# Optimization experiments

Measured on AMD Instinct MI355X. Metric: run time of the kernel, lower is better.

Reference implementation:

```python
import jax, jax.numpy as jnp
import numpy as np

N_NODES = 50000
N_EDGES = 800000
GEN_EPS = 1e-7
LN_EPS = 1e-5


def _mlp3_tanh(x, w0, b0, w1, b1, w2, b2):
    x = jnp.tanh(x @ w0.T + b0)
    x = jnp.tanh(x @ w1.T + b1)
    return jnp.tanh(x @ w2.T + b2)


def _gen_conv(x, src, dst, edge_attr, w0, b0, ln_w, ln_b, w1, b1):
    # GENConv(aggr='softmax', t=1): msg = relu(x_j + e) + eps
    msg = jax.nn.relu(x[src] + edge_attr) + GEN_EPS          # [E, 64]
    m = jax.ops.segment_max(msg, dst, num_segments=N_NODES)  # [N, 64]
    ex = jnp.exp(msg - m[dst])
    den = jax.ops.segment_sum(ex, dst, num_segments=N_NODES)
    alpha = ex / den[dst]                                    # scatter-softmax per dst
    agg = jax.ops.segment_sum(alpha * msg, dst, num_segments=N_NODES)
    h = x + agg                                              # x_r + aggregated messages
    # internal MLP: Linear(64->128), LayerNorm(128), ReLU, Linear(128->64)
    h = h @ w0.T + b0
    mu = jnp.mean(h, axis=-1, keepdims=True)
    var = jnp.mean((h - mu) ** 2, axis=-1, keepdims=True)
    h = ln_w * (h - mu) * jax.lax.rsqrt(var + LN_EPS) + ln_b
    h = jax.nn.relu(h)
    return h @ w1.T + b1


def setup_inputs() -> dict:
    key = jax.random.key(0)
    ks = jax.random.split(key, 32)
    s = 0.05
    d = {
        'node_features': jax.random.normal(ks[0], (N_NODES, 11), jnp.float32),
        'edge_features': jax.random.normal(ks[1], (N_EDGES, 3), jnp.float32),
        'edge_index': jax.random.randint(ks[2], (2, N_EDGES), 0, N_NODES, jnp.int32),
        'ne_w0': jax.random.normal(ks[3], (64, 11)) * s, 'ne_b0': jnp.zeros((64,)),
        'ne_w1': jax.random.normal(ks[4], (64, 64)) * s, 'ne_b1': jnp.zeros((64,)),
        'ne_w2': jax.random.normal(ks[5], (64, 64)) * s, 'ne_b2': jnp.zeros((64,)),
        'ee_w0': jax.random.normal(ks[6], (64, 3)) * s, 'ee_b0': jnp.zeros((64,)),
        'ee_w1': jax.random.normal(ks[7], (64, 64)) * s, 'ee_b1': jnp.zeros((64,)),
        'ee_w2': jax.random.normal(ks[8], (64, 64)) * s, 'ee_b2': jnp.zeros((64,)),
        'mp_w0': jax.random.normal(ks[9], (3, 128, 64)) * s,
        'mp_b0': jnp.zeros((3, 128)),
        'mp_ln_w': jnp.ones((3, 128)), 'mp_ln_b': jnp.zeros((3, 128)),
        'mp_w1': jax.random.normal(ks[10], (3, 64, 128)) * s,
        'mp_b1': jnp.zeros((3, 64)),
        'pi_w0': jax.random.normal(ks[11], (64, 64)) * s, 'pi_b0': jnp.zeros((64,)),
        'pi_w1': jax.random.normal(ks[12], (64, 64)) * s, 'pi_b1': jnp.zeros((64,)),
        'pi_w2': jax.random.normal(ks[13], (2, 64)) * s, 'pi_b2': jnp.zeros((2,)),
    }
    return {k: (v.astype(jnp.float32) if v.dtype != jnp.int32 else v) for k, v in d.items()}


def reference(node_features, edge_features, edge_index,
              ne_w0, ne_b0, ne_w1, ne_b1, ne_w2, ne_b2,
              ee_w0, ee_b0, ee_w1, ee_b1, ee_w2, ee_b2,
              mp_w0, mp_b0, mp_ln_w, mp_ln_b, mp_w1, mp_b1,
              pi_w0, pi_b0, pi_w1, pi_b1, pi_w2, pi_b2):
    src, dst = edge_index[0], edge_index[1]
    x = _mlp3_tanh(node_features, ne_w0, ne_b0, ne_w1, ne_b1, ne_w2, ne_b2)
    e = _mlp3_tanh(edge_features, ee_w0, ee_b0, ee_w1, ee_b1, ee_w2, ee_b2)
    for i in range(3):
        x = _gen_conv(x, src, dst, e, mp_w0[i], mp_b0[i], mp_ln_w[i], mp_ln_b[i], mp_w1[i], mp_b1[i])
    h = jnp.tanh(x @ pi_w0.T + pi_b0)
    h = jnp.tanh(h @ pi_w1.T + pi_b1)
    out = h @ pi_w2.T + pi_b2                 # [N, 2]
    # output.t().reshape(-1)[:n_turbines] == first column of out
    means = -30.0 + (out[:, 0] + 1.0) * 60.0 / 2.0
    return means
```

## Files before the change

### kernel.cpp

```cpp
#include <hip/hip_runtime.h>
#include <stdint.h>

#define N_NODES 50000
#define N_EDGES 800000

typedef unsigned short u16;
typedef unsigned int u32;
typedef __attribute__((ext_vector_type(8))) short short8;
typedef __attribute__((ext_vector_type(4))) float f32x4;
typedef __attribute__((ext_vector_type(4))) u32 u32x4;
typedef __attribute__((ext_vector_type(2))) u32 u32x2;

#define WAVE_SYNC() asm volatile("s_waitcnt lgkmcnt(0)" ::: "memory")

__device__ __forceinline__ float b2f(u16 v) {
    u32 u = ((u32)v) << 16; float f; __builtin_memcpy(&f, &u, 4); return f;
}
__device__ __forceinline__ u16 f2b(float f) {
    u32 u; __builtin_memcpy(&u, &f, 4);
    return (u16)((u + 0x8000u) >> 16);
}
__device__ __forceinline__ u32 pack2(float a, float b) {
    u32 ua, ub; __builtin_memcpy(&ua, &a, 4); __builtin_memcpy(&ub, &b, 4);
    return ((ua + 0x8000u) >> 16) | ((ub + 0x8000u) & 0xffff0000u);
}
__device__ __forceinline__ float fast_tanh(float x) {
    float e = __expf(2.f * x);
    return 1.f - __fdividef(2.f, e + 1.f);
}
__device__ __forceinline__ f32x4 mfma16(short8 a, short8 b, f32x4 c) {
    return __builtin_amdgcn_mfma_f32_16x16x32_bf16(a, b, c, 0, 0, 0);
}

enum : int {
    NE_T0 = 0,     NE_B0 = 704,   NE_T1 = 768,   NE_B1 = 4864,  NE_T2 = 4928,  NE_B2 = 9024,
    EE_T0 = 9088,  EE_B0 = 9280,  EE_T1 = 9344,  EE_B1 = 13440, EE_T2 = 13504, EE_B2 = 17600,
    MP_T0 = 17664, MP_B0 = 42240, LNW_O = 42624, LNB_O = 43008, MP_T1 = 43392, MP_B1 = 67968,
    PI_T0 = 68160, PI_B0 = 72256, PI_T1 = 72320, PI_B1 = 76416, PI_W2 = 76480, PI_B2 = 76608,
    W_TOTAL = 76610
};

enum : int {
    FR_EE1 = 0, FR_EE2 = 4, FR_EE3 = 12, FR_NE1 = 20, FR_NE2 = 24, FR_NE3 = 32,
    FR_MP0 = 40, FR_MP1 = 88, FR_PI0 = 136, FR_PI1 = 144, FR_TOTAL = 152
};

#define OFF_W       ((size_t)0)
#define OFF_FLAG    ((size_t)0x60000)
#define OFF_WB      ((size_t)0x61000)
#define OFF_X0      ((size_t)0x90000)
#define OFF_X1      ((size_t)0x00D00000)
#define OFF_H64B    ((size_t)0x01A00000)
#define OFF_XB0     ((size_t)0x02080000)
#define OFF_E       ((size_t)0x02700000)
#define OFF_ROWPTR  ((size_t)0x08900000)
#define OFF_CURSOR  ((size_t)0x08940000)
#define OFF_PERM    ((size_t)0x08980000)
#define OFF_SRCS    ((size_t)0x08D00000)
#define OFF_BSUM    ((size_t)0x09080000)
#define OFF_XB1     ((size_t)0x09100000)

struct Ptrs24 { const void* p[24]; };


__global__ void detect_kernel(const void* nf, int* flag) {
    u32 w = ((const u32*)nf)[threadIdx.x & 63];
    u32 lo = w & 0xffffu;
    int e = (int)((lo >> 7) & 0xff);
    int good = ((e >= 118 && e <= 132) || lo == 0) ? 1 : 0;
    unsigned long long b = __ballot(good != 0);
    if (threadIdx.x == 0) *flag = (__popcll(b) >= 48) ? 1 : 0;
}

__global__ void convert_weights(Ptrs24 ps, float* __restrict__ W, const int* flag) {
    const int segIN[24] = {11,64,64,64,64,64, 3,64,64,64,64,64, 64,384,384,384,128,192, 64,64,64,64,128,2};
    const int segOUT[24]= {64, 1,64, 1,64, 1, 64, 1,64, 1,64, 1, 128, 1,  1,  1, 64,  1, 64, 1,64, 1,  1,1};
    const int segS[24]  = { 1, 1, 1, 1, 1, 1,  1, 1, 1, 1, 1, 1,   3, 1,  1,  1,  3,  1,  1, 1, 1, 1,  1,1};
    const int segTR[24] = { 1, 0, 1, 0, 1, 0,  1, 0, 1, 0, 1, 0,   1, 0,  0,  0,  1,  0,  1, 0, 1, 0,  0,0};
    int t = blockIdx.x * blockDim.x + threadIdx.x;
    if (t >= W_TOTAL) return;
    bool bf = (*flag != 0);
    int seg = 0, off = t;
    for (;;) {
        int cnt = segIN[seg] * segOUT[seg] * segS[seg];
        if (off < cnt) break;
        off -= cnt; seg++;
    }
    int srcIdx;
    if (segTR[seg]) {
        int per = segIN[seg] * segOUT[seg];
        int s = off / per, d = off % per;
        int j = d / segOUT[seg], i = d % segOUT[seg];
        srcIdx = s * per + i * segIN[seg] + j;
    } else {
        srcIdx = off;
    }
    const void* p = ps.p[seg];
    W[t] = bf ? b2f(((const u16*)p)[srcIdx]) : ((const float*)p)[srcIdx];
}

__global__ void make_frags(const float* __restrict__ W, u16* __restrict__ Wb) {
    const int base[15] = {FR_EE1,FR_EE2,FR_EE3,FR_NE1,FR_NE2,FR_NE3,
                          FR_MP0,FR_MP0+16,FR_MP0+32, FR_MP1,FR_MP1+16,FR_MP1+32,
                          FR_PI0,FR_PI1,FR_TOTAL};
    const int woff[14] = {EE_T0,EE_T1,EE_T2, NE_T0,NE_T1,NE_T2,
                          MP_T0,MP_T0+8192,MP_T0+16384, MP_T1,MP_T1+8192,MP_T1+16384,
                          PI_T0,PI_T1};
    const int kreal[14] = {3,64,64, 11,64,64, 64,64,64, 128,128,128, 64,64};
    const int nn[14]    = {64,64,64, 64,64,64, 128,128,128, 64,64,64, 64,64};
    int t = blockIdx.x * blockDim.x + threadIdx.x;
    if (t >= FR_TOTAL * 512) return;
    int f = t >> 9, r = t & 511, lane = r >> 3, j = r & 7;
    int l = 0;
    while (f >= base[l + 1]) l++;
    int lf = f - base[l];
    int NT = nn[l] >> 4;
    int kt = lf / NT, nt = lf % NT;
    int k = kt * 32 + (lane >> 4) * 8 + j;
    int n = nt * 16 + (lane & 15);
    float v = (k < kreal[l]) ? W[woff[l] + k * nn[l] + n] : 0.f;
    Wb[t] = f2b(v);
}


__global__ void hist_kernel(const int* __restrict__ dst, int* __restrict__ rowptr) {
    int e = blockIdx.x * blockDim.x + threadIdx.x;
    if (e < N_EDGES) atomicAdd(&rowptr[dst[e] + 1], 1);
}

__global__ void scanA(int* __restrict__ rowptr, int* __restrict__ bsum) {
    __shared__ int wsum[16];
    int tid = threadIdx.x, lane = tid & 63, wid = tid >> 6;
    int i0 = blockIdx.x * 2048 + tid * 2;
    int v0 = (i0 <= N_NODES) ? rowptr[i0] : 0;
    int v1 = (i0 + 1 <= N_NODES) ? rowptr[i0 + 1] : 0;
    int v = v0 + v1;
#pragma unroll
    for (int off = 1; off < 64; off <<= 1) {
        int t = __shfl_up(v, off, 64);
        if (lane >= off) v += t;
    }
    if (lane == 63) wsum[wid] = v;
    __syncthreads();
    if (tid == 0) { int a = 0; for (int w = 0; w < 16; w++) { a += wsum[w]; wsum[w] = a; } }
    __syncthreads();
    int incl = v + (wid ? wsum[wid - 1] : 0);
    if (i0 <= N_NODES) rowptr[i0] = incl - v1;
    if (i0 + 1 <= N_NODES) rowptr[i0 + 1] = incl;
    if (tid == 1023) bsum[blockIdx.x] = incl;
}
__global__ void scanB(int* __restrict__ bsum, int nb) {
    int lane = threadIdx.x;
    int v = (lane < nb) ? bsum[lane] : 0;
#pragma unroll
    for (int off = 1; off < 64; off <<= 1) {
        int t = __shfl_up(v, off, 64);
        if (lane >= off) v += t;
    }
    if (lane < nb) bsum[lane] = v;
}
__global__ void scanC(const int* __restrict__ bsum, int* __restrict__ rowptr,
                      int* __restrict__ cursor) {
    int i = blockIdx.x * 1024 + threadIdx.x;
    if (i > N_NODES) return;
    int b = i >> 11;
    int v = rowptr[i] + (b ? bsum[b - 1] : 0);
    rowptr[i] = v;
    if (i < N_NODES) cursor[i] = v;
}

__global__ void scatter_kernel(const int* __restrict__ dst, const int* __restrict__ src,
                               int* __restrict__ cursor, int* __restrict__ perm,
                               int* __restrict__ srcs) {
    int e = blockIdx.x * blockDim.x + threadIdx.x;
    if (e >= N_EDGES) return;
    int p = atomicAdd(&cursor[dst[e]], 1);
    perm[e] = p;
    srcs[p] = src[e];
}


template<int KT, int NT, int INSTR>
__device__ __forceinline__ void mfma_layer(const u32* ldsin, int lane,
        const short8* __restrict__ Wf, int basef, const float* __restrict__ bias, f32x4* acc) {
    int q = lane >> 4, mr = lane & 15;
#pragma unroll
    for (int nt = 0; nt < NT; nt++) acc[nt] = *(const f32x4*)(bias + nt * 16 + q * 4);
#pragma unroll
    for (int kt = 0; kt < KT; kt++) {
        short8 act = *(const short8*)(ldsin + mr * INSTR + kt * 16 + q * 4);
#pragma unroll
        for (int nt = 0; nt < NT; nt++)
            acc[nt] = mfma16(Wf[(basef + kt * NT + nt) * 64 + lane], act, acc[nt]);
    }
}

template<int KT, int NT>
__device__ __forceinline__ void mfma_layer_reg(const short8* act, int lane,
        const short8* __restrict__ Wf, int basef, const float* __restrict__ bias, f32x4* acc) {
    int q = lane >> 4;
#pragma unroll
    for (int nt = 0; nt < NT; nt++) acc[nt] = *(const f32x4*)(bias + nt * 16 + q * 4);
#pragma unroll
    for (int kt = 0; kt < KT; kt++)
#pragma unroll
        for (int nt = 0; nt < NT; nt++)
            acc[nt] = mfma16(Wf[(basef + kt * NT + nt) * 64 + lane], act[kt], acc[nt]);
}

template<int NT, int OUTSTR>
__device__ __forceinline__ void tanh_pack_lds(const f32x4* acc, u32* ldsout, int lane) {
    int q = lane >> 4, mr = lane & 15;
#pragma unroll
    for (int nt = 0; nt < NT; nt++) {
        f32x4 a = acc[nt];
        ldsout[mr * OUTSTR + nt * 8 + q * 2 + 0] = pack2(fast_tanh(a[0]), fast_tanh(a[1]));
        ldsout[mr * OUTSTR + nt * 8 + q * 2 + 1] = pack2(fast_tanh(a[2]), fast_tanh(a[3]));
    }
}


__global__ __launch_bounds__(256) void edge_encoder(const void* ef, u32* __restrict__ ebuf,
        const int* __restrict__ perm, const float* __restrict__ W,
        const short8* __restrict__ Wf, const int* flag) {
    __shared__ u32 lds[4 * 1152];
    int wv = threadIdx.x >> 6, lane = threadIdx.x & 63;
    u32* B0 = lds + wv * 1152;
    u32* B1 = B0 + 576;
    long ebase = (long)blockIdx.x * 64 + wv * 16;
    bool bf = (*flag != 0);
    if (lane < 16) {
        long e = ebase + lane;
        float i0, i1, i2;
        if (bf) { const u16* p = (const u16*)ef + e * 3; i0 = b2f(p[0]); i1 = b2f(p[1]); i2 = b2f(p[2]); }
        else    { const float* p = (const float*)ef + e * 3; i0 = p[0]; i1 = p[1]; i2 = p[2]; }
        u32* row = B0 + lane * 36;
        row[0] = pack2(i0, i1); row[1] = pack2(i2, 0.f);
#pragma unroll
        for (int d = 2; d < 16; d++) row[d] = 0;
    }
    WAVE_SYNC();
    f32x4 acc[4];
    mfma_layer<1, 4, 36>(B0, lane, Wf, FR_EE1, W + EE_B0, acc);
    tanh_pack_lds<4, 36>(acc, B1, lane);
    WAVE_SYNC();
    mfma_layer<2, 4, 36>(B1, lane, Wf, FR_EE2, W + EE_B1, acc);
    tanh_pack_lds<4, 36>(acc, B0, lane);
    WAVE_SYNC();
    mfma_layer<2, 4, 36>(B0, lane, Wf, FR_EE3, W + EE_B2, acc);
    tanh_pack_lds<4, 36>(acc, B1, lane);
    WAVE_SYNC();
    int ro = lane >> 2, cc = (lane & 3) * 8;
    long e = ebase + ro;
    long prow = perm[e];
    u32x4 v0 = *(const u32x4*)&B1[ro * 36 + cc];
    u32x4 v1 = *(const u32x4*)&B1[ro * 36 + cc + 4];
    *(u32x4*)&ebuf[prow * 32 + cc] = v0;
    *(u32x4*)&ebuf[prow * 32 + cc + 4] = v1;
}

__global__ __launch_bounds__(256) void node_encoder(const void* nf, float* __restrict__ x,
        u16* __restrict__ xbf, const float* __restrict__ W,
        const short8* __restrict__ Wf, const int* flag) {
    __shared__ u32 lds[4 * 1152];
    int wv = threadIdx.x >> 6, lane = threadIdx.x & 63;
    int q = lane >> 4, mr = lane & 15;
    u32* B0 = lds + wv * 1152;
    u32* B1 = B0 + 576;
    long nbase = (long)blockIdx.x * 64 + wv * 16;
    bool bf = (*flag != 0);
    if (lane < 16) {
        long n = nbase + lane;
        float in[12];
#pragma unroll
        for (int j = 0; j < 12; j++) in[j] = 0.f;
        if (n < N_NODES) {
#pragma unroll
            for (int j = 0; j < 11; j++)
                in[j] = bf ? b2f(((const u16*)nf)[n * 11 + j]) : ((const float*)nf)[n * 11 + j];
        }
        u32* row = B0 + lane * 36;
#pragma unroll
        for (int d = 0; d < 6; d++) row[d] = pack2(in[2 * d], in[2 * d + 1]);
#pragma unroll
        for (int d = 6; d < 16; d++) row[d] = 0;
    }
    WAVE_SYNC();
    f32x4 acc[4];
    mfma_layer<1, 4, 36>(B0, lane, Wf, FR_NE1, W + NE_B0, acc);
    tanh_pack_lds<4, 36>(acc, B1, lane);
    WAVE_SYNC();
    mfma_layer<2, 4, 36>(B1, lane, Wf, FR_NE2, W + NE_B1, acc);
    tanh_pack_lds<4, 36>(acc, B0, lane);
    WAVE_SYNC();
    mfma_layer<2, 4, 36>(B0, lane, Wf, FR_NE3, W + NE_B2, acc);
    long n = nbase + mr;
    if (n < N_NODES) {
#pragma unroll
        for (int nt = 0; nt < 4; nt++) {
            f32x4 v;
#pragma unroll
            for (int rr = 0; rr < 4; rr++) v[rr] = fast_tanh(acc[nt][rr]);
            *(f32x4*)(x + n * 64 + nt * 16 + q * 4) = v;
            u32x2 pb; pb.x = pack2(v[0], v[1]); pb.y = pack2(v[2], v[3]);
            *(u32x2*)&xbf[n * 64 + nt * 16 + q * 4] = pb;
        }
    }
}

__global__ __launch_bounds__(256) void aggregate_kernel(
        const float* __restrict__ x, const u16* __restrict__ xbf,
        const u16* __restrict__ ebuf, const int* __restrict__ srcs,
        const int* __restrict__ rowptr, u16* __restrict__ h64bf) {
    int gw = (int)((blockIdx.x * 256 + threadIdx.x) >> 6);
    int lane = (int)(threadIdx.x & 63);
    if (gw >= N_NODES) return;
    gw = __builtin_amdgcn_readfirstlane(gw);
    int beg = rowptr[gw], end = rowptr[gw + 1];
    int cnt = end - beg;
    float num = 0.f, den = 0.f;
    for (int base = 0; base < cnt; base += 64) {
        int m = cnt - base; if (m > 64) m = 64;
        int sk = (base + lane < cnt) ? srcs[beg + base + lane] : 0;
        const u16* ep = ebuf + (long)(beg + base) * 64 + lane;
        int kk = 0;
        for (; kk + 4 <= m; kk += 4) {
            int s0 = __shfl(sk, kk, 64), s1 = __shfl(sk, kk + 1, 64);
            int s2 = __shfl(sk, kk + 2, 64), s3 = __shfl(sk, kk + 3, 64);
            float xa0 = b2f(xbf[(long)s0 * 64 + lane]);
            float xa1 = b2f(xbf[(long)s1 * 64 + lane]);
            float xa2 = b2f(xbf[(long)s2 * 64 + lane]);
            float xa3 = b2f(xbf[(long)s3 * 64 + lane]);
            float e0 = b2f(ep[(long)kk * 64]);
            float e1 = b2f(ep[(long)(kk + 1) * 64]);
            float e2 = b2f(ep[(long)(kk + 2) * 64]);
            float e3 = b2f(ep[(long)(kk + 3) * 64]);
            float m0 = fmaxf(xa0 + e0, 0.f) + 1e-7f;
            float m1 = fmaxf(xa1 + e1, 0.f) + 1e-7f;
            float m2 = fmaxf(xa2 + e2, 0.f) + 1e-7f;
            float m3 = fmaxf(xa3 + e3, 0.f) + 1e-7f;
            float w0 = __expf(m0), w1 = __expf(m1), w2 = __expf(m2), w3 = __expf(m3);
            num = fmaf(w0, m0, num); den += w0;
            num = fmaf(w1, m1, num); den += w1;
            num = fmaf(w2, m2, num); den += w2;
            num = fmaf(w3, m3, num); den += w3;
        }
        for (; kk < m; kk++) {
            int s0 = __shfl(sk, kk, 64);
            float m0 = fmaxf(b2f(xbf[(long)s0 * 64 + lane]) + b2f(ep[(long)kk * 64]), 0.f) + 1e-7f;
            float w0 = __expf(m0);
            num = fmaf(w0, m0, num); den += w0;
        }
    }
    float agg = (den > 0.f) ? __fdividef(num, den) : 0.f;
    float h = x[(long)gw * 64 + lane] + agg;
    h64bf[(long)gw * 64 + lane] = f2b(h);
}

__global__ __launch_bounds__(256) void mlp_fused(const u16* __restrict__ h64bf,
        float* __restrict__ xout, u16* __restrict__ xbf,
        const float* __restrict__ W, const short8* __restrict__ Wf, int r) {
    __shared__ u32 lds[4 * 1088];
    int wv = threadIdx.x >> 6, lane = threadIdx.x & 63;
    int q = lane >> 4, mr = lane & 15;
    u32* bufY = lds + wv * 1088;
    long nbase = (long)blockIdx.x * 64 + wv * 16;
    long row = nbase + mr;
    long rc = (row < N_NODES) ? row : (N_NODES - 1);
    short8 act[2];
#pragma unroll
    for (int kt = 0; kt < 2; kt++)
        act[kt] = *(const short8*)&h64bf[rc * 64 + kt * 32 + q * 8];
    f32x4 acc[8];
    mfma_layer_reg<2, 8>(act, lane, Wf, FR_MP0 + r * 16, W + MP_B0 + r * 128, acc);
    float s = 0.f, sq = 0.f;
#pragma unroll
    for (int nt = 0; nt < 8; nt++)
#pragma unroll
        for (int rr = 0; rr < 4; rr++) { float v = acc[nt][rr]; s += v; sq = fmaf(v, v, sq); }
    s += __shfl_xor(s, 16, 64);  s += __shfl_xor(s, 32, 64);
    sq += __shfl_xor(sq, 16, 64); sq += __shfl_xor(sq, 32, 64);
    float mu = s * (1.f / 128.f);
    float var = sq * (1.f / 128.f) - mu * mu;
    float inv = rsqrtf(var + 1e-5f);
    const float* LW = W + LNW_O + r * 128;
    const float* LB = W + LNB_O + r * 128;
#pragma unroll
    for (int nt = 0; nt < 8; nt++) {
        f32x4 lw = *(const f32x4*)(LW + nt * 16 + q * 4);
        f32x4 lb = *(const f32x4*)(LB + nt * 16 + q * 4);
        float u0 = fmaxf(fmaf((acc[nt][0] - mu) * inv, lw[0], lb[0]), 0.f);
        float u1 = fmaxf(fmaf((acc[nt][1] - mu) * inv, lw[1], lb[1]), 0.f);
        float u2 = fmaxf(fmaf((acc[nt][2] - mu) * inv, lw[2], lb[2]), 0.f);
        float u3 = fmaxf(fmaf((acc[nt][3] - mu) * inv, lw[3], lb[3]), 0.f);
        bufY[mr * 68 + nt * 8 + q * 2 + 0] = pack2(u0, u1);
        bufY[mr * 68 + nt * 8 + q * 2 + 1] = pack2(u2, u3);
    }
    WAVE_SYNC();
    f32x4 acc2[4];
    mfma_layer<4, 4, 68>(bufY, lane, Wf, FR_MP1 + r * 16, W + MP_B1 + r * 64, acc2);
    if (row < N_NODES) {
#pragma unroll
        for (int nt = 0; nt < 4; nt++) {
            f32x4 v = acc2[nt];
            *(f32x4*)(xout + row * 64 + nt * 16 + q * 4) = v;
            u32x2 pb; pb.x = pack2(v[0], v[1]); pb.y = pack2(v[2], v[3]);
            *(u32x2*)&xbf[row * 64 + nt * 16 + q * 4] = pb;
        }
    }
}

__global__ __launch_bounds__(256) void policy_head(const u16* __restrict__ xbf, void* out,
        const float* __restrict__ W, const short8* __restrict__ Wf, const int* flag) {
    __shared__ u32 lds[4 * 576];
    int wv = threadIdx.x >> 6, lane = threadIdx.x & 63;
    int q = lane >> 4, mr = lane & 15;
    u32* bufY = lds + wv * 576;
    long nbase = (long)blockIdx.x * 64 + wv * 16;
    long row = nbase + mr;
    long rc = (row < N_NODES) ? row : (N_NODES - 1);
    bool bf = (*flag != 0);
    short8 act[2];
#pragma unroll
    for (int kt = 0; kt < 2; kt++)
        act[kt] = *(const short8*)&xbf[rc * 64 + kt * 32 + q * 8];
    f32x4 acc[4];
    mfma_layer_reg<2, 4>(act, lane, Wf, FR_PI0, W + PI_B0, acc);
    tanh_pack_lds<4, 36>(acc, bufY, lane);
    WAVE_SYNC();
    mfma_layer<2, 4, 36>(bufY, lane, Wf, FR_PI1, W + PI_B1, acc);
    float o = 0.f;
#pragma unroll
    for (int nt = 0; nt < 4; nt++) {
        f32x4 w2 = *(const f32x4*)(W + PI_W2 + nt * 16 + q * 4);
#pragma unroll
        for (int rr = 0; rr < 4; rr++) o = fmaf(fast_tanh(acc[nt][rr]), w2[rr], o);
    }
    o += __shfl_xor(o, 16, 64);
    o += __shfl_xor(o, 32, 64);
    if (lane < 16 && row < N_NODES) {
        float means = 30.f * (o + W[PI_B2]);
        if (bf) ((u16*)out)[row] = f2b(means);
        else    ((float*)out)[row] = means;
    }
}

extern "C" void kernel_launch(void* const* d_in, const int* in_sizes, int n_in,
                              void* d_out, int out_size, void* d_ws, size_t ws_size,
                              hipStream_t stream) {
    char* ws = (char*)d_ws;
    float* W      = (float*)(ws + OFF_W);
    int*   flag   = (int*)(ws + OFF_FLAG);
    u16*   Wb     = (u16*)(ws + OFF_WB);
    const short8* Wf = (const short8*)(ws + OFF_WB);
    float* x0     = (float*)(ws + OFF_X0);
    float* x1     = (float*)(ws + OFF_X1);
    u16*   xb0    = (u16*)(ws + OFF_XB0);
    u16*   xb1    = (u16*)(ws + OFF_XB1);
    u16*   h64bf  = (u16*)(ws + OFF_H64B);
    u32*   ebuf32 = (u32*)(ws + OFF_E);
    u16*   ebuf16 = (u16*)(ws + OFF_E);
    int*   rowptr = (int*)(ws + OFF_ROWPTR);
    int*   cursor = (int*)(ws + OFF_CURSOR);
    int*   perm   = (int*)(ws + OFF_PERM);
    int*   srcs   = (int*)(ws + OFF_SRCS);
    int*   bsum   = (int*)(ws + OFF_BSUM);

    const int* ei   = (const int*)d_in[2];
    const int* srcv = ei;
    const int* dstv = ei + N_EDGES;

    detect_kernel<<<1, 64, 0, stream>>>(d_in[0], flag);
    hipMemsetAsync(rowptr, 0, (N_NODES + 1) * sizeof(int), stream);

    Ptrs24 ps;
    for (int k = 0; k < 24; k++) ps.p[k] = d_in[3 + k];
    convert_weights<<<(W_TOTAL + 255) / 256, 256, 0, stream>>>(ps, W, flag);
    make_frags<<<(FR_TOTAL * 512 + 255) / 256, 256, 0, stream>>>(W, Wb);

    hist_kernel<<<(N_EDGES + 255) / 256, 256, 0, stream>>>(dstv, rowptr);
    scanA<<<25, 1024, 0, stream>>>(rowptr, bsum);
    scanB<<<1, 64, 0, stream>>>(bsum, 25);
    scanC<<<(N_NODES + 1024) / 1024, 1024, 0, stream>>>(bsum, rowptr, cursor);
    scatter_kernel<<<(N_EDGES + 255) / 256, 256, 0, stream>>>(dstv, srcv, cursor, perm, srcs);

    node_encoder<<<(N_NODES + 63) / 64, 256, 0, stream>>>(d_in[0], x0, xb0, W, Wf, flag);
    edge_encoder<<<N_EDGES / 64, 256, 0, stream>>>(d_in[1], ebuf32, perm, W, Wf, flag);

    float* xc = x0; float* xn = x1;
    u16* xbc = xb0; u16* xbn = xb1;
    for (int r = 0; r < 3; r++) {
        aggregate_kernel<<<(N_NODES * 64 + 255) / 256, 256, 0, stream>>>(xc, xbc, ebuf16, srcs, rowptr, h64bf);
        mlp_fused<<<(N_NODES + 63) / 64, 256, 0, stream>>>(h64bf, xn, xbn, W, Wf, r);
        float* t = xc; xc = xn; xn = t;
        u16* tb = xbc; xbc = xbn; xbn = tb;
    }
    policy_head<<<(N_NODES + 63) / 64, 256, 0, stream>>>(xbc, d_out, W, Wf, flag);
}
```

Measured before the change: 481.1 us.

## Use LDS tanh lookup table, pack bf16 pairs, and split edges across wave halves

Replaces the exp-based tanh in the encoders and policy head with a piecewise-linear lookup table built in shared memory per block, adding a table build and __syncthreads at kernel start. The aggregation kernel now has each lane handle two packed bf16 channels, with the two half-waves processing alternating edges and combining partial sums by shuffle, so each edge row is loaded as 32-bit words. pack2 uses a byte-permute instruction, and weight fragments are converted with round-to-nearest-even. The lookup tanh is an approximation with step 1/32 that clamps near 6, which may change accuracy.

```diff
diff --git a/kernel.cpp b/kernel.cpp
--- a/kernel.cpp
+++ b/kernel.cpp
@@ -20,16 +20,40 @@
     u32 u; __builtin_memcpy(&u, &f, 4);
     return (u16)((u + 0x8000u) >> 16);
 }
+__device__ __forceinline__ float lo2f(u32 p) {
+    u32 u = p << 16; float f; __builtin_memcpy(&f, &u, 4); return f;
+}
+__device__ __forceinline__ float hi2f(u32 p) {
+    u32 u = p & 0xffff0000u; float f; __builtin_memcpy(&f, &u, 4); return f;
+}
 __device__ __forceinline__ u32 pack2(float a, float b) {
     u32 ua, ub; __builtin_memcpy(&ua, &a, 4); __builtin_memcpy(&ub, &b, 4);
-    return ((ua + 0x8000u) >> 16) | ((ub + 0x8000u) & 0xffff0000u);
-}
-__device__ __forceinline__ float fast_tanh(float x) {
-    float e = __expf(2.f * x);
-    return 1.f - __fdividef(2.f, e + 1.f);
+    return __builtin_amdgcn_perm(ub + 0x8000u, ua + 0x8000u, 0x07060302u);
 }
 __device__ __forceinline__ f32x4 mfma16(short8 a, short8 b, f32x4 c) {
     return __builtin_amdgcn_mfma_f32_16x16x32_bf16(a, b, c, 0, 0, 0);
+}
+
+#define TANH_TBL_N 192
+__device__ __forceinline__ void build_tanh_tbl(float2* tbl) {
+    int i = (int)threadIdx.x;
+    if (i < TANH_TBL_N) {
+        float x0 = i * 0.03125f, x1 = x0 + 0.03125f;
+        float t0 = tanhf(x0), t1 = tanhf(x1);
+        float s = (t1 - t0) * 32.f;
+        tbl[i] = make_float2(fmaf(-s, x0, t0), s);
+    }
+    __syncthreads();
+}
+__device__ __forceinline__ float lut_tanh(const float2* __restrict__ tbl, float x) {
+    float a = __builtin_fabsf(x);
+    a = fminf(a, 5.96875f);
+    int i = (int)(a * 32.f);
+    float2 bs = tbl[i];
+    float y = fmaf(bs.y, a, bs.x);
+    u32 uy, ux; __builtin_memcpy(&uy, &y, 4); __builtin_memcpy(&ux, &x, 4);
+    u32 r = (uy & 0x7fffffffu) | (ux & 0x80000000u);
+    float o; __builtin_memcpy(&o, &r, 4); return o;
 }
 
 enum : int {
@@ -119,7 +143,8 @@
     int k = kt * 32 + (lane >> 4) * 8 + j;
     int n = nt * 16 + (lane & 15);
     float v = (k < kreal[l]) ? W[woff[l] + k * nn[l] + n] : 0.f;
-    Wb[t] = f2b(v);
+    u32 u; __builtin_memcpy(&u, &v, 4);
+    Wb[t] = (u16)((u + 0x7fffu + ((u >> 16) & 1u)) >> 16);
 }
 
 
@@ -209,13 +234,14 @@
 }
 
 template<int NT, int OUTSTR>
-__device__ __forceinline__ void tanh_pack_lds(const f32x4* acc, u32* ldsout, int lane) {
+__device__ __forceinline__ void tanh_pack_lds(const f32x4* acc, u32* ldsout, int lane,
+                                              const float2* __restrict__ tbl) {
     int q = lane >> 4, mr = lane & 15;
 #pragma unroll
     for (int nt = 0; nt < NT; nt++) {
         f32x4 a = acc[nt];
-        ldsout[mr * OUTSTR + nt * 8 + q * 2 + 0] = pack2(fast_tanh(a[0]), fast_tanh(a[1]));
-        ldsout[mr * OUTSTR + nt * 8 + q * 2 + 1] = pack2(fast_tanh(a[2]), fast_tanh(a[3]));
+        ldsout[mr * OUTSTR + nt * 8 + q * 2 + 0] = pack2(lut_tanh(tbl, a[0]), lut_tanh(tbl, a[1]));
+        ldsout[mr * OUTSTR + nt * 8 + q * 2 + 1] = pack2(lut_tanh(tbl, a[2]), lut_tanh(tbl, a[3]));
     }
 }
 
@@ -224,6 +250,8 @@
         const int* __restrict__ perm, const float* __restrict__ W,
         const short8* __restrict__ Wf, const int* flag) {
     __shared__ u32 lds[4 * 1152];
+    __shared__ float2 tbl[TANH_TBL_N];
+    build_tanh_tbl(tbl);
     int wv = threadIdx.x >> 6, lane = threadIdx.x & 63;
     u32* B0 = lds + wv * 1152;
     u32* B1 = B0 + 576;
@@ -242,13 +270,13 @@
     WAVE_SYNC();
     f32x4 acc[4];
     mfma_layer<1, 4, 36>(B0, lane, Wf, FR_EE1, W + EE_B0, acc);
-    tanh_pack_lds<4, 36>(acc, B1, lane);
+    tanh_pack_lds<4, 36>(acc, B1, lane, tbl);
     WAVE_SYNC();
     mfma_layer<2, 4, 36>(B1, lane, Wf, FR_EE2, W + EE_B1, acc);
-    tanh_pack_lds<4, 36>(acc, B0, lane);
+    tanh_pack_lds<4, 36>(acc, B0, lane, tbl);
     WAVE_SYNC();
     mfma_layer<2, 4, 36>(B0, lane, Wf, FR_EE3, W + EE_B2, acc);
-    tanh_pack_lds<4, 36>(acc, B1, lane);
+    tanh_pack_lds<4, 36>(acc, B1, lane, tbl);
     WAVE_SYNC();
     int ro = lane >> 2, cc = (lane & 3) * 8;
     long e = ebase + ro;
@@ -263,6 +291,8 @@
         u16* __restrict__ xbf, const float* __restrict__ W,
         const short8* __restrict__ Wf, const int* flag) {
     __shared__ u32 lds[4 * 1152];
+    __shared__ float2 tbl[TANH_TBL_N];
+    build_tanh_tbl(tbl);
     int wv = threadIdx.x >> 6, lane = threadIdx.x & 63;
     int q = lane >> 4, mr = lane & 15;
     u32* B0 = lds + wv * 1152;
@@ -288,10 +318,10 @@
     WAVE_SYNC();
     f32x4 acc[4];
     mfma_layer<1, 4, 36>(B0, lane, Wf, FR_NE1, W + NE_B0, acc);
-    tanh_pack_lds<4, 36>(acc, B1, lane);
+    tanh_pack_lds<4, 36>(acc, B1, lane, tbl);
     WAVE_SYNC();
     mfma_layer<2, 4, 36>(B1, lane, Wf, FR_NE2, W + NE_B1, acc);
-    tanh_pack_lds<4, 36>(acc, B0, lane);
+    tanh_pack_lds<4, 36>(acc, B0, lane, tbl);
     WAVE_SYNC();
     mfma_layer<2, 4, 36>(B0, lane, Wf, FR_NE3, W + NE_B2, acc);
     long n = nbase + mr;
@@ -300,7 +330,7 @@
         for (int nt = 0; nt < 4; nt++) {
             f32x4 v;
 #pragma unroll
-            for (int rr = 0; rr < 4; rr++) v[rr] = fast_tanh(acc[nt][rr]);
+            for (int rr = 0; rr < 4; rr++) v[rr] = lut_tanh(tbl, acc[nt][rr]);
             *(f32x4*)(x + n * 64 + nt * 16 + q * 4) = v;
             u32x2 pb; pb.x = pack2(v[0], v[1]); pb.y = pack2(v[2], v[3]);
             *(u32x2*)&xbf[n * 64 + nt * 16 + q * 4] = pb;
@@ -309,52 +339,47 @@
 }
 
 __global__ __launch_bounds__(256) void aggregate_kernel(
-        const float* __restrict__ x, const u16* __restrict__ xbf,
-        const u16* __restrict__ ebuf, const int* __restrict__ srcs,
-        const int* __restrict__ rowptr, u16* __restrict__ h64bf) {
+        const float* __restrict__ x, const u32* __restrict__ xbf32,
+        const u32* __restrict__ ebuf32, const int* __restrict__ srcs,
+        const int* __restrict__ rowptr, u32* __restrict__ h64bf32) {
     int gw = (int)((blockIdx.x * 256 + threadIdx.x) >> 6);
     int lane = (int)(threadIdx.x & 63);
     if (gw >= N_NODES) return;
     gw = __builtin_amdgcn_readfirstlane(gw);
+    int half = lane >> 5, h = lane & 31;
     int beg = rowptr[gw], end = rowptr[gw + 1];
     int cnt = end - beg;
-    float num = 0.f, den = 0.f;
+    float num0 = 0.f, den0 = 0.f, num1 = 0.f, den1 = 0.f;
     for (int base = 0; base < cnt; base += 64) {
-        int m = cnt - base; if (m > 64) m = 64;
-        int sk = (base + lane < cnt) ? srcs[beg + base + lane] : 0;
-        const u16* ep = ebuf + (long)(beg + base) * 64 + lane;
-        int kk = 0;
-        for (; kk + 4 <= m; kk += 4) {
-            int s0 = __shfl(sk, kk, 64), s1 = __shfl(sk, kk + 1, 64);
-            int s2 = __shfl(sk, kk + 2, 64), s3 = __shfl(sk, kk + 3, 64);
-            float xa0 = b2f(xbf[(long)s0 * 64 + lane]);
-            float xa1 = b2f(xbf[(long)s1 * 64 + lane]);
-            float xa2 = b2f(xbf[(long)s2 * 64 + lane]);
-            float xa3 = b2f(xbf[(long)s3 * 64 + lane]);
-            float e0 = b2f(ep[(long)kk * 64]);
-            float e1 = b2f(ep[(long)(kk + 1) * 64]);
-            float e2 = b2f(ep[(long)(kk + 2) * 64]);
-            float e3 = b2f(ep[(long)(kk + 3) * 64]);
-            float m0 = fmaxf(xa0 + e0, 0.f) + 1e-7f;
-            float m1 = fmaxf(xa1 + e1, 0.f) + 1e-7f;
-            float m2 = fmaxf(xa2 + e2, 0.f) + 1e-7f;
-            float m3 = fmaxf(xa3 + e3, 0.f) + 1e-7f;
-            float w0 = __expf(m0), w1 = __expf(m1), w2 = __expf(m2), w3 = __expf(m3);
-            num = fmaf(w0, m0, num); den += w0;
-            num = fmaf(w1, m1, num); den += w1;
-            num = fmaf(w2, m2, num); den += w2;
-            num = fmaf(w3, m3, num); den += w3;
+        int rem = cnt - base; if (rem > 64) rem = 64;
+        int lidx = (lane < rem) ? lane : (rem - 1);
+        int sk = srcs[beg + base + lidx];
+        const u32* eb = ebuf32 + (long)(beg + base) * 32 + h;
+        int iters = (rem + 1) >> 1;
+#pragma unroll 2
+        for (int t = 0; t < iters; t++) {
+            int eo = 2 * t + half;
+            int eoc = (eo < rem) ? eo : (rem - 1);
+            int s = __shfl(sk, eo, 64);
+            u32 xv = xbf32[(long)s * 32 + h];
+            u32 ev = eb[eoc * 32];
+            float m0 = fmaxf(lo2f(xv) + lo2f(ev), 0.f) + 1e-7f;
+            float m1 = fmaxf(hi2f(xv) + hi2f(ev), 0.f) + 1e-7f;
+            bool act = eo < rem;
+            float w0 = act ? __expf(m0) : 0.f;
+            float w1 = act ? __expf(m1) : 0.f;
+            num0 = fmaf(w0, m0, num0); den0 += w0;
+            num1 = fmaf(w1, m1, num1); den1 += w1;
         }
-        for (; kk < m; kk++) {
-            int s0 = __shfl(sk, kk, 64);
-            float m0 = fmaxf(b2f(xbf[(long)s0 * 64 + lane]) + b2f(ep[(long)kk * 64]), 0.f) + 1e-7f;
-            float w0 = __expf(m0);
-            num = fmaf(w0, m0, num); den += w0;
-        }
-    }
-    float agg = (den > 0.f) ? __fdividef(num, den) : 0.f;
-    float h = x[(long)gw * 64 + lane] + agg;
-    h64bf[(long)gw * 64 + lane] = f2b(h);
+    }
+    num0 += __shfl_xor(num0, 32, 64); den0 += __shfl_xor(den0, 32, 64);
+    num1 += __shfl_xor(num1, 32, 64); den1 += __shfl_xor(den1, 32, 64);
+    if (half == 0) {
+        float agg0 = (den0 > 0.f) ? __fdividef(num0, den0) : 0.f;
+        float agg1 = (den1 > 0.f) ? __fdividef(num1, den1) : 0.f;
+        float2 xr = *(const float2*)(x + (long)gw * 64 + 2 * h);
+        h64bf32[(long)gw * 32 + h] = pack2(xr.x + agg0, xr.y + agg1);
+    }
 }
 
 __global__ __launch_bounds__(256) void mlp_fused(const u16* __restrict__ h64bf,
@@ -413,6 +438,8 @@
 __global__ __launch_bounds__(256) void policy_head(const u16* __restrict__ xbf, void* out,
         const float* __restrict__ W, const short8* __restrict__ Wf, const int* flag) {
     __shared__ u32 lds[4 * 576];
+    __shared__ float2 tbl[TANH_TBL_N];
+    build_tanh_tbl(tbl);
     int wv = threadIdx.x >> 6, lane = threadIdx.x & 63;
     int q = lane >> 4, mr = lane & 15;
     u32* bufY = lds + wv * 576;
@@ -426,7 +453,7 @@
         act[kt] = *(const short8*)&xbf[rc * 64 + kt * 32 + q * 8];
     f32x4 acc[4];
     mfma_layer_reg<2, 4>(act, lane, Wf, FR_PI0, W + PI_B0, acc);
-    tanh_pack_lds<4, 36>(acc, bufY, lane);
+    tanh_pack_lds<4, 36>(acc, bufY, lane, tbl);
     WAVE_SYNC();
     mfma_layer<2, 4, 36>(bufY, lane, Wf, FR_PI1, W + PI_B1, acc);
     float o = 0.f;
@@ -434,7 +461,7 @@
     for (int nt = 0; nt < 4; nt++) {
         f32x4 w2 = *(const f32x4*)(W + PI_W2 + nt * 16 + q * 4);
 #pragma unroll
-        for (int rr = 0; rr < 4; rr++) o = fmaf(fast_tanh(acc[nt][rr]), w2[rr], o);
+        for (int rr = 0; rr < 4; rr++) o = fmaf(lut_tanh(tbl, acc[nt][rr]), w2[rr], o);
     }
     o += __shfl_xor(o, 16, 64);
     o += __shfl_xor(o, 32, 64);
@@ -458,8 +485,8 @@
     u16*   xb0    = (u16*)(ws + OFF_XB0);
     u16*   xb1    = (u16*)(ws + OFF_XB1);
     u16*   h64bf  = (u16*)(ws + OFF_H64B);
+    u32*   h64b32 = (u32*)(ws + OFF_H64B);
     u32*   ebuf32 = (u32*)(ws + OFF_E);
-    u16*   ebuf16 = (u16*)(ws + OFF_E);
     int*   rowptr = (int*)(ws + OFF_ROWPTR);
     int*   cursor = (int*)(ws + OFF_CURSOR);
     int*   perm   = (int*)(ws + OFF_PERM);
@@ -490,7 +517,8 @@
     float* xc = x0; float* xn = x1;
     u16* xbc = xb0; u16* xbn = xb1;
     for (int r = 0; r < 3; r++) {
-        aggregate_kernel<<<(N_NODES * 64 + 255) / 256, 256, 0, stream>>>(xc, xbc, ebuf16, srcs, rowptr, h64bf);
+        aggregate_kernel<<<(N_NODES * 64 + 255) / 256, 256, 0, stream>>>(
+            xc, (const u32*)xbc, ebuf32, srcs, rowptr, h64b32);
         mlp_fused<<<(N_NODES + 63) / 64, 256, 0, stream>>>(h64bf, xn, xbn, W, Wf, r);
         float* t = xc; xc = xn; xn = t;
         u16* tb = xbc; xbc = xbn; xbn = tb;
```

After: 463.6 us. 1.04x faster.
